# Optimization experiments

Hardware: AMD Instinct MI355X
Metric: run time of the kernel (lower is better)

Reference implementation:

```python
import jax, jax.numpy as jnp
import numpy as np

N_NODES = 1000000
N_EDGES = 32000000
NUM_GRAPHS = 1024


def setup_inputs() -> dict:
    key = jax.random.key(0)
    k1, k2, k3, k4, k5 = jax.random.split(key, 5)
    x = jax.random.normal(k1, (N_NODES, 1), dtype=jnp.float32)
    W = jax.random.normal(k2, (1, 1), dtype=jnp.float32)
    b = jax.random.normal(k3, (1,), dtype=jnp.float32)
    edge_index = jax.random.randint(k4, (2, N_EDGES), 0, N_NODES, dtype=jnp.int64)
    batch = jnp.sort(jax.random.randint(k5, (N_NODES,), 0, NUM_GRAPHS, dtype=jnp.int64))
    return {"x": x, "W": W, "b": b, "edge_index": edge_index, "batch": batch}


def reference(x, W, b, edge_index, batch):
    src, dst = edge_index[0], edge_index[1]
    # SimpleConv (default sum aggregation): out[i] = sum_{(j->i) in E} x[j]
    agg = jax.ops.segment_sum(x[src], dst, num_segments=N_NODES)  # [N,1]
    h = jax.nn.relu(agg)
    # global_mean_pool over graph ids
    sums = jax.ops.segment_sum(h, batch, num_segments=NUM_GRAPHS)  # [G,1]
    counts = jax.ops.segment_sum(jnp.ones((N_NODES,), dtype=h.dtype), batch,
                                 num_segments=NUM_GRAPHS)  # [G]
    pooled = sums / jnp.maximum(counts, 1.0)[:, None]
    # Linear(1 -> 1): y = pooled @ W^T + b
    return pooled @ W.T + b
```

## Files before the change

### kernel.cpp

```cpp
#include <hip/hip_runtime.h>

#define N_NODES    1000000
#define N_EDGES    32000000
#define NUM_GRAPHS 1024

typedef int          vint4  __attribute__((ext_vector_type(4)));
typedef unsigned int uint32;
typedef unsigned int vuint4 __attribute__((ext_vector_type(4)));

#define BUCKET_SHIFT 12
#define BUCKET_NODES (1 << BUCKET_SHIFT)
#define NBUCKETS     245

#define T1_NCHUNK   512
#define T1_BLOCK    512
#define T1_EDGES_PER_CHUNK (N_EDGES / T1_NCHUNK)
#define T1_QUADS    (T1_EDGES_PER_CHUNK / 4)
#define T1_ROUNDS   ((T1_QUADS + T1_BLOCK - 1) / T1_BLOCK)
#define SCAP        64
#define SLAB_CAP    368

#define RSPLIT        4
#define CELLS_PER_WG  (T1_NCHUNK / RSPLIT)

#define T2_CAP      136192
#define T2_NCHUNK   512
#define T2_EPC      (N_EDGES / T2_NCHUNK)

__global__ __launch_bounds__(T1_BLOCK)
void slab_scatter(const int* __restrict__ src,
                  const int* __restrict__ dst,
                  uint32* __restrict__ slab,
                  uint32* __restrict__ fcnt_g,
                  uint32* __restrict__ ecnt_g) {
    __shared__ uint32 stage[NBUCKETS][SCAP];
    __shared__ uint32 rpos[NBUCKETS];
    __shared__ uint32 ecnt[NBUCKETS];
    __shared__ uint32 flushed[NBUCKETS];
    __shared__ uint32 carry[NBUCKETS];

    const int tid = threadIdx.x;
    const int w   = blockIdx.x;
    const vint4* d4 = (const vint4*)(dst + (size_t)w * T1_EDGES_PER_CHUNK);
    const vint4* s4 = (const vint4*)(src + (size_t)w * T1_EDGES_PER_CHUNK);

    for (int b = tid; b < NBUCKETS; b += T1_BLOCK) {
        rpos[b] = 0; ecnt[b] = 0; flushed[b] = 0; carry[b] = 0;
    }
    __syncthreads();

    const int grp    = tid >> 4;
    const int lane16 = tid & 15;

    for (int r = 0; r < T1_ROUNDS; ++r) {
        int q = r * T1_BLOCK + tid;
        if (q < T1_QUADS) {
            vint4 d = d4[q];
            vint4 s = s4[q];
            #pragma unroll
            for (int k = 0; k < 4; ++k) {
                uint32 dd = (uint32)(k == 0 ? d.x : k == 1 ? d.y : k == 2 ? d.z : d.w);
                uint32 ss = (uint32)(k == 0 ? s.x : k == 1 ? s.y : k == 2 ? s.z : s.w);
                uint32 b  = dd >> BUCKET_SHIFT;
                uint32 v  = ((dd & (BUCKET_NODES - 1)) << 20) | ss;
                uint32 c  = carry[b] + atomicAdd(&rpos[b], 1u);
                if (c < SCAP) {
                    stage[b][c] = v;
                } else {
                    uint32 e = atomicAdd(&ecnt[b], 1u);
                    slab[((size_t)b * T1_NCHUNK + w) * SLAB_CAP + (SLAB_CAP - 1 - e)] = v;
                }
            }
        }
        __syncthreads();
        for (int b = grp; b < NBUCKETS; b += 32) {
            uint32 tot = carry[b] + rpos[b];
            if (tot > SCAP) tot = SCAP;
            uint32 lines = tot >> 4;
            uint32 rem   = tot & 15u;
            uint32 fl    = flushed[b];
            uint32* dp = slab + ((size_t)b * T1_NCHUNK + w) * SLAB_CAP + fl;
            for (uint32 l = 0; l < lines; ++l)
                dp[l * 16 + lane16] = stage[b][l * 16 + lane16];
            if (lines) {
                uint32 mv = 0;
                if (lane16 < rem) mv = stage[b][lines * 16 + lane16];
                if (lane16 < rem) stage[b][lane16] = mv;
            }
            if (lane16 == 0) {
                flushed[b] = fl + lines * 16;
                carry[b]   = rem;
                rpos[b]    = 0;
            }
        }
        __syncthreads();
    }
    for (int b = grp; b < NBUCKETS; b += 32) {
        uint32 rem = carry[b];
        uint32 fl  = flushed[b];
        uint32* dp = slab + ((size_t)b * T1_NCHUNK + w) * SLAB_CAP + fl;
        if (lane16 < rem) dp[lane16] = stage[b][lane16];
        if (lane16 == 0) {
            fcnt_g[(size_t)b * T1_NCHUNK + w] = fl + rem;
            ecnt_g[(size_t)b * T1_NCHUNK + w] = ecnt[b];
        }
    }
}

__global__ __launch_bounds__(1024)
void slab_reduce2(const uint32* __restrict__ slab,
                  const uint32* __restrict__ fcnt_g,
                  const uint32* __restrict__ ecnt_g,
                  const float* __restrict__ x,
                  float* __restrict__ agg) {
    __shared__ float  acc[BUCKET_NODES];
    __shared__ uint32 fc_s[CELLS_PER_WG];
    __shared__ uint32 ec_s[CELLS_PER_WG];

    const int b    = blockIdx.x / RSPLIT;
    const int part = blockIdx.x % RSPLIT;
    const int tid  = threadIdx.x;

    for (int n = tid; n < BUCKET_NODES; n += 1024) acc[n] = 0.0f;
    if (tid < CELLS_PER_WG) {
        size_t cell = (size_t)b * T1_NCHUNK + (size_t)part * CELLS_PER_WG + tid;
        fc_s[tid] = fcnt_g[cell];
        ec_s[tid] = ecnt_g[cell];
    }
    __syncthreads();

    const int wv = tid >> 6, lane = tid & 63;
    for (int c = wv; c < CELLS_PER_WG; c += 16) {
        const int w = part * CELLS_PER_WG + c;
        const size_t cell = (size_t)b * T1_NCHUNK + w;
        const uint32 fc = fc_s[c];
        const uint32 ec = ec_s[c];
        const uint32* base = slab + cell * SLAB_CAP;
        const vuint4* b4 = (const vuint4*)base;
        const uint32 nq = fc >> 2;
        for (uint32 i = lane; i < nq; i += 64) {
            vuint4 v = __builtin_nontemporal_load(&b4[i]);
            atomicAdd(&acc[v.x >> 20], x[v.x & 0xFFFFFu]);
            atomicAdd(&acc[v.y >> 20], x[v.y & 0xFFFFFu]);
            atomicAdd(&acc[v.z >> 20], x[v.z & 0xFFFFFu]);
            atomicAdd(&acc[v.w >> 20], x[v.w & 0xFFFFFu]);
        }
        for (uint32 i = nq * 4 + lane; i < fc; i += 64) {
            uint32 v = __builtin_nontemporal_load(&base[i]);
            atomicAdd(&acc[v >> 20], x[v & 0xFFFFFu]);
        }
        for (uint32 i = lane; i < ec; i += 64) {
            uint32 v = base[SLAB_CAP - 1 - i];
            atomicAdd(&acc[v >> 20], x[v & 0xFFFFFu]);
        }
    }
    __syncthreads();

    const int node0 = b << BUCKET_SHIFT;
    for (int n = tid; n < BUCKET_NODES; n += 1024) {
        float v = acc[n];
        if (v != 0.0f) atomicAdd(&agg[node0 + n], v);
    }
}

__global__ __launch_bounds__(1024)
void slab_reduce(const uint32* __restrict__ slab,
                 const uint32* __restrict__ fcnt_g,
                 const uint32* __restrict__ ecnt_g,
                 const float* __restrict__ x,
                 const int* __restrict__ batch,
                 float* __restrict__ sums,
                 float* __restrict__ counts) {
    __shared__ float acc[BUCKET_NODES];
    const int b = blockIdx.x;
    const int tid = threadIdx.x;
    for (int n = tid; n < BUCKET_NODES; n += 1024) acc[n] = 0.0f;
    __syncthreads();

    const int wv = tid >> 6, lane = tid & 63;
    for (int w = wv; w < T1_NCHUNK; w += 16) {
        size_t cell = (size_t)b * T1_NCHUNK + w;
        uint32 fc = fcnt_g[cell];
        uint32 ec = ecnt_g[cell];
        const uint32* base = slab + cell * SLAB_CAP;
        const vuint4* b4 = (const vuint4*)base;
        uint32 nq = fc >> 2;
        for (uint32 i = lane; i < nq; i += 64) {
            vuint4 v = b4[i];
            atomicAdd(&acc[v.x >> 20], x[v.x & 0xFFFFFu]);
            atomicAdd(&acc[v.y >> 20], x[v.y & 0xFFFFFu]);
            atomicAdd(&acc[v.z >> 20], x[v.z & 0xFFFFFu]);
            atomicAdd(&acc[v.w >> 20], x[v.w & 0xFFFFFu]);
        }
        for (uint32 i = nq * 4 + lane; i < fc; i += 64) {
            uint32 v = base[i];
            atomicAdd(&acc[v >> 20], x[v & 0xFFFFFu]);
        }
        for (uint32 i = lane; i < ec; i += 64) {
            uint32 v = base[SLAB_CAP - 1 - i];
            atomicAdd(&acc[v >> 20], x[v & 0xFFFFFu]);
        }
    }
    __syncthreads();

    const int node0 = b << BUCKET_SHIFT;
    for (int n = tid; n < BUCKET_NODES; n += 1024) {
        int i = node0 + n;
        float h = 0.0f;
        int g = -1;
        if (i < N_NODES) {
            h = fmaxf(acc[n], 0.0f);
            g = batch[i];
        }
        int g0 = __shfl(g, 0);
        if (__all(g == g0)) {
            #pragma unroll
            for (int off = 32; off > 0; off >>= 1)
                h += __shfl_down(h, off);
            if ((tid & 63) == 0 && g0 >= 0) {
                atomicAdd(&sums[g0], h);
                atomicAdd(&counts[g0], 64.0f);
            }
        } else if (g >= 0) {
            atomicAdd(&sums[g], h);
            atomicAdd(&counts[g], 1.0f);
        }
    }
}

__global__ void finalize_kernel(const float* __restrict__ sums,
                                const float* __restrict__ counts,
                                const float* __restrict__ W,
                                const float* __restrict__ b,
                                float* __restrict__ out) {
    int g = blockIdx.x * blockDim.x + threadIdx.x;
    if (g < NUM_GRAPHS) {
        float pooled = sums[g] / fmaxf(counts[g], 1.0f);
        out[g] = pooled * W[0] + b[0];
    }
}

__global__ __launch_bounds__(1024)
void bucket_scatter(const int* __restrict__ src,
                    const int* __restrict__ dst,
                    uint32* __restrict__ sorted,
                    uint32* __restrict__ gpos) {
    __shared__ uint32 hist[NBUCKETS];
    __shared__ uint32 pos[NBUCKETS];
    const int tid = threadIdx.x;
    const size_t base = (size_t)blockIdx.x * T2_EPC;
    for (int b = tid; b < NBUCKETS; b += 1024) hist[b] = 0;
    __syncthreads();
    const vint4* d4 = (const vint4*)(dst + base);
    const vint4* s4 = (const vint4*)(src + base);
    const int nvec = T2_EPC / 4;
    for (int i = tid; i < nvec; i += 1024) {
        vint4 d = d4[i];
        atomicAdd(&hist[(uint32)d.x >> BUCKET_SHIFT], 1u);
        atomicAdd(&hist[(uint32)d.y >> BUCKET_SHIFT], 1u);
        atomicAdd(&hist[(uint32)d.z >> BUCKET_SHIFT], 1u);
        atomicAdd(&hist[(uint32)d.w >> BUCKET_SHIFT], 1u);
    }
    __syncthreads();
    for (int b = tid; b < NBUCKETS; b += 1024)
        pos[b] = atomicAdd(&gpos[b], hist[b]);
    __syncthreads();
    for (int i = tid; i < nvec; i += 1024) {
        vint4 d = d4[i];
        vint4 s = s4[i];
        #pragma unroll
        for (int k = 0; k < 4; ++k) {
            uint32 dd = (uint32)(k == 0 ? d.x : k == 1 ? d.y : k == 2 ? d.z : d.w);
            uint32 ss = (uint32)(k == 0 ? s.x : k == 1 ? s.y : k == 2 ? s.z : s.w);
            uint32 b = dd >> BUCKET_SHIFT, dl = dd & (BUCKET_NODES - 1);
            uint32 slot = atomicAdd(&pos[b], 1u);
            if (slot < T2_CAP) sorted[(size_t)b * T2_CAP + slot] = (dl << 20) | ss;
        }
    }
}

__global__ __launch_bounds__(1024)
void bucket_reduce(const uint32* __restrict__ sorted,
                   const uint32* __restrict__ gpos,
                   const float* __restrict__ x,
                   const int* __restrict__ batch,
                   float* __restrict__ sums,
                   float* __restrict__ counts) {
    __shared__ float acc[BUCKET_NODES];
    const int b = blockIdx.x;
    const int tid = threadIdx.x;
    for (int n = tid; n < BUCKET_NODES; n += 1024) acc[n] = 0.0f;
    __syncthreads();
    uint32 cnt = gpos[b];
    if (cnt > T2_CAP) cnt = T2_CAP;
    const uint32* reg = sorted + (size_t)b * T2_CAP;
    const vuint4* r4 = (const vuint4*)reg;
    const uint32 nvec = cnt / 4;
    for (uint32 i = tid; i < nvec; i += 1024) {
        vuint4 v = r4[i];
        atomicAdd(&acc[v.x >> 20], x[v.x & 0xFFFFFu]);
        atomicAdd(&acc[v.y >> 20], x[v.y & 0xFFFFFu]);
        atomicAdd(&acc[v.z >> 20], x[v.z & 0xFFFFFu]);
        atomicAdd(&acc[v.w >> 20], x[v.w & 0xFFFFFu]);
    }
    for (uint32 i = nvec * 4 + tid; i < cnt; i += 1024) {
        uint32 v = reg[i];
        atomicAdd(&acc[v >> 20], x[v & 0xFFFFFu]);
    }
    __syncthreads();
    const int node0 = b << BUCKET_SHIFT;
    for (int n = tid; n < BUCKET_NODES; n += 1024) {
        int i = node0 + n;
        float h = 0.0f;
        int g = -1;
        if (i < N_NODES) {
            h = fmaxf(acc[n], 0.0f);
            g = batch[i];
        }
        int g0 = __shfl(g, 0);
        if (__all(g == g0)) {
            #pragma unroll
            for (int off = 32; off > 0; off >>= 1)
                h += __shfl_down(h, off);
            if ((tid & 63) == 0 && g0 >= 0) {
                atomicAdd(&sums[g0], h);
                atomicAdd(&counts[g0], 64.0f);
            }
        } else if (g >= 0) {
            atomicAdd(&sums[g], h);
            atomicAdd(&counts[g], 1.0f);
        }
    }
}

__global__ void scatter_edges_dev(const vint4* __restrict__ src4,
                                  const vint4* __restrict__ dst4,
                                  const float* __restrict__ x,
                                  float* __restrict__ agg) {
    int t = blockIdx.x * blockDim.x + threadIdx.x;
    if (t < N_EDGES / 4) {
        vint4 s = __builtin_nontemporal_load(&src4[t]);
        vint4 d = __builtin_nontemporal_load(&dst4[t]);
        atomicAdd(&agg[d.x], x[s.x]);
        atomicAdd(&agg[d.y], x[s.y]);
        atomicAdd(&agg[d.z], x[s.z]);
        atomicAdd(&agg[d.w], x[s.w]);
    }
}

__global__ void pool_nodes_kernel(const float* __restrict__ agg,
                                  const int* __restrict__ batch,
                                  float* __restrict__ sums,
                                  float* __restrict__ counts) {
    int i = blockIdx.x * blockDim.x + threadIdx.x;
    float h = 0.0f;
    int g = -1;
    if (i < N_NODES) {
        h = fmaxf(agg[i], 0.0f);
        g = batch[i];
    }
    int g0 = __shfl(g, 0);
    if (__all(g == g0)) {
        #pragma unroll
        for (int off = 32; off > 0; off >>= 1)
            h += __shfl_down(h, off);
        if ((threadIdx.x & 63) == 0 && g0 >= 0) {
            atomicAdd(&sums[g0], h);
            atomicAdd(&counts[g0], 64.0f);
        }
    } else if (g >= 0) {
        atomicAdd(&sums[g], h);
        atomicAdd(&counts[g], 1.0f);
    }
}

extern "C" void kernel_launch(void* const* d_in, const int* in_sizes, int n_in,
                              void* d_out, int out_size, void* d_ws, size_t ws_size,
                              hipStream_t stream) {
    const float* x     = (const float*)d_in[0];
    const float* W     = (const float*)d_in[1];
    const float* b     = (const float*)d_in[2];
    const int*   edge  = (const int*)d_in[3];
    const int*   batch = (const int*)d_in[4];
    float* out = (float*)d_out;

    const int* src = edge;
    const int* dst = edge + N_EDGES;

    const size_t ncells     = (size_t)NBUCKETS * T1_NCHUNK;
    const size_t slab_elems = ncells * SLAB_CAP;
    const size_t nagg       = (size_t)NBUCKETS * BUCKET_NODES;
    const size_t need0 = (slab_elems + 2 * ncells + nagg + 2 * NUM_GRAPHS) * 4;
    const size_t need1 = (slab_elems + 2 * ncells + 2 * NUM_GRAPHS) * 4;
    const size_t t2_elems = (size_t)NBUCKETS * T2_CAP;
    const size_t need2 = (t2_elems + 256 + 2 * NUM_GRAPHS) * 4;

    if (ws_size >= need0) {
        uint32* slab   = (uint32*)d_ws;
        uint32* fcnt_g = slab + slab_elems;
        uint32* ecnt_g = fcnt_g + ncells;
        float*  agg    = (float*)(ecnt_g + ncells);
        float*  sums   = agg + nagg;
        float*  counts = sums + NUM_GRAPHS;
        (void)hipMemsetAsync(agg, 0, (nagg + 2 * NUM_GRAPHS) * 4, stream);

        slab_scatter<<<T1_NCHUNK, T1_BLOCK, 0, stream>>>(src, dst, slab, fcnt_g, ecnt_g);
        slab_reduce2<<<NBUCKETS * RSPLIT, 1024, 0, stream>>>(slab, fcnt_g, ecnt_g, x, agg);
        pool_nodes_kernel<<<(N_NODES + 255) / 256, 256, 0, stream>>>(agg, batch, sums, counts);
        finalize_kernel<<<(NUM_GRAPHS + 255) / 256, 256, 0, stream>>>(sums, counts, W, b, out);
    } else if (ws_size >= need1) {
        uint32* slab   = (uint32*)d_ws;
        uint32* fcnt_g = slab + slab_elems;
        uint32* ecnt_g = fcnt_g + ncells;
        float*  sums   = (float*)(ecnt_g + ncells);
        float*  counts = sums + NUM_GRAPHS;
        (void)hipMemsetAsync(sums, 0, 2 * NUM_GRAPHS * 4, stream);

        slab_scatter<<<T1_NCHUNK, T1_BLOCK, 0, stream>>>(src, dst, slab, fcnt_g, ecnt_g);
        slab_reduce<<<NBUCKETS, 1024, 0, stream>>>(slab, fcnt_g, ecnt_g, x, batch, sums, counts);
        finalize_kernel<<<(NUM_GRAPHS + 255) / 256, 256, 0, stream>>>(sums, counts, W, b, out);
    } else if (ws_size >= need2) {
        uint32* sorted = (uint32*)d_ws;
        uint32* gpos   = sorted + t2_elems;
        float*  sums   = (float*)(gpos + 256);
        float*  counts = sums + NUM_GRAPHS;
        (void)hipMemsetAsync(gpos, 0, (256 + 2 * NUM_GRAPHS) * 4, stream);

        bucket_scatter<<<T2_NCHUNK, 1024, 0, stream>>>(src, dst, sorted, gpos);
        bucket_reduce<<<NBUCKETS, 1024, 0, stream>>>(sorted, gpos, x, batch, sums, counts);
        finalize_kernel<<<(NUM_GRAPHS + 255) / 256, 256, 0, stream>>>(sums, counts, W, b, out);
    } else {
        float* agg    = (float*)d_ws;
        float* sums   = agg + N_NODES;
        float* counts = sums + NUM_GRAPHS;
        (void)hipMemsetAsync(d_ws, 0, ((size_t)N_NODES + 2 * NUM_GRAPHS) * 4, stream);

        int nthreads = N_EDGES / 4;
        scatter_edges_dev<<<(nthreads + 255) / 256, 256, 0, stream>>>(
            (const vint4*)src, (const vint4*)dst, x, agg);
        pool_nodes_kernel<<<(N_NODES + 255) / 256, 256, 0, stream>>>(agg, batch, sums, counts);
        finalize_kernel<<<(NUM_GRAPHS + 255) / 256, 256, 0, stream>>>(sums, counts, W, b, out);
    }
}
```

Measured before the change: 650.1 us.

## Split reduce by source-node halves and use nontemporal loads/stores in scatter

The reduce kernel launches twice as many workgroups. Each one reads the whole slab cell but only gathers x values whose source index falls in its half of the node range, which shrinks the working set of x each workgroup touches so the random gathers stay in cache better. The scatter kernel switches its edge loads and slab stores to nontemporal hints so streaming traffic does not evict cached data. In exchange, every slab entry is now read twice and the extra range-check branches add divergence.

Result: slower. 692.5 us (+6.5%).

```diff
diff --git a/kernel.cpp b/kernel.cpp
--- a/kernel.cpp
+++ b/kernel.cpp
@@ -22,6 +22,8 @@
 
 #define RSPLIT        4
 #define CELLS_PER_WG  (T1_NCHUNK / RSPLIT)
+#define SRC_SPLIT     2
+#define HALF_NODES    (N_NODES / SRC_SPLIT)
 
 #define T2_CAP      136192
 #define T2_NCHUNK   512
@@ -55,8 +57,8 @@
     for (int r = 0; r < T1_ROUNDS; ++r) {
         int q = r * T1_BLOCK + tid;
         if (q < T1_QUADS) {
-            vint4 d = d4[q];
-            vint4 s = s4[q];
+            vint4 d = __builtin_nontemporal_load(&d4[q]);
+            vint4 s = __builtin_nontemporal_load(&s4[q]);
             #pragma unroll
             for (int k = 0; k < 4; ++k) {
                 uint32 dd = (uint32)(k == 0 ? d.x : k == 1 ? d.y : k == 2 ? d.z : d.w);
@@ -68,7 +70,8 @@
                     stage[b][c] = v;
                 } else {
                     uint32 e = atomicAdd(&ecnt[b], 1u);
-                    slab[((size_t)b * T1_NCHUNK + w) * SLAB_CAP + (SLAB_CAP - 1 - e)] = v;
+                    __builtin_nontemporal_store(v,
+                        &slab[((size_t)b * T1_NCHUNK + w) * SLAB_CAP + (SLAB_CAP - 1 - e)]);
                 }
             }
         }
@@ -81,7 +84,8 @@
             uint32 fl    = flushed[b];
             uint32* dp = slab + ((size_t)b * T1_NCHUNK + w) * SLAB_CAP + fl;
             for (uint32 l = 0; l < lines; ++l)
-                dp[l * 16 + lane16] = stage[b][l * 16 + lane16];
+                __builtin_nontemporal_store(stage[b][l * 16 + lane16],
+                                            &dp[l * 16 + lane16]);
             if (lines) {
                 uint32 mv = 0;
                 if (lane16 < rem) mv = stage[b][lines * 16 + lane16];
@@ -99,7 +103,7 @@
         uint32 rem = carry[b];
         uint32 fl  = flushed[b];
         uint32* dp = slab + ((size_t)b * T1_NCHUNK + w) * SLAB_CAP + fl;
-        if (lane16 < rem) dp[lane16] = stage[b][lane16];
+        if (lane16 < rem) __builtin_nontemporal_store(stage[b][lane16], &dp[lane16]);
         if (lane16 == 0) {
             fcnt_g[(size_t)b * T1_NCHUNK + w] = fl + rem;
             ecnt_g[(size_t)b * T1_NCHUNK + w] = ecnt[b];
@@ -117,9 +121,14 @@
     __shared__ uint32 fc_s[CELLS_PER_WG];
     __shared__ uint32 ec_s[CELLS_PER_WG];
 
-    const int b    = blockIdx.x / RSPLIT;
-    const int part = blockIdx.x % RSPLIT;
+    const int half = blockIdx.x & 1;
+    const int rest = blockIdx.x >> 1;
+    const int b    = rest / RSPLIT;
+    const int part = rest % RSPLIT;
     const int tid  = threadIdx.x;
+
+    const uint32 lo = (uint32)half * HALF_NODES;
+    const uint32 hi = lo + HALF_NODES;
 
     for (int n = tid; n < BUCKET_NODES; n += 1024) acc[n] = 0.0f;
     if (tid < CELLS_PER_WG) {
@@ -140,18 +149,22 @@
         const uint32 nq = fc >> 2;
         for (uint32 i = lane; i < nq; i += 64) {
             vuint4 v = __builtin_nontemporal_load(&b4[i]);
-            atomicAdd(&acc[v.x >> 20], x[v.x & 0xFFFFFu]);
-            atomicAdd(&acc[v.y >> 20], x[v.y & 0xFFFFFu]);
-            atomicAdd(&acc[v.z >> 20], x[v.z & 0xFFFFFu]);
-            atomicAdd(&acc[v.w >> 20], x[v.w & 0xFFFFFu]);
+            uint32 s0 = v.x & 0xFFFFFu, s1 = v.y & 0xFFFFFu;
+            uint32 s2 = v.z & 0xFFFFFu, s3 = v.w & 0xFFFFFu;
+            if (s0 >= lo && s0 < hi) atomicAdd(&acc[v.x >> 20], x[s0]);
+            if (s1 >= lo && s1 < hi) atomicAdd(&acc[v.y >> 20], x[s1]);
+            if (s2 >= lo && s2 < hi) atomicAdd(&acc[v.z >> 20], x[s2]);
+            if (s3 >= lo && s3 < hi) atomicAdd(&acc[v.w >> 20], x[s3]);
         }
         for (uint32 i = nq * 4 + lane; i < fc; i += 64) {
             uint32 v = __builtin_nontemporal_load(&base[i]);
-            atomicAdd(&acc[v >> 20], x[v & 0xFFFFFu]);
+            uint32 s = v & 0xFFFFFu;
+            if (s >= lo && s < hi) atomicAdd(&acc[v >> 20], x[s]);
         }
         for (uint32 i = lane; i < ec; i += 64) {
             uint32 v = base[SLAB_CAP - 1 - i];
-            atomicAdd(&acc[v >> 20], x[v & 0xFFFFFu]);
+            uint32 s = v & 0xFFFFFu;
+            if (s >= lo && s < hi) atomicAdd(&acc[v >> 20], x[s]);
         }
     }
     __syncthreads();
@@ -405,7 +418,8 @@
         (void)hipMemsetAsync(agg, 0, (nagg + 2 * NUM_GRAPHS) * 4, stream);
 
         slab_scatter<<<T1_NCHUNK, T1_BLOCK, 0, stream>>>(src, dst, slab, fcnt_g, ecnt_g);
-        slab_reduce2<<<NBUCKETS * RSPLIT, 1024, 0, stream>>>(slab, fcnt_g, ecnt_g, x, agg);
+        slab_reduce2<<<NBUCKETS * RSPLIT * SRC_SPLIT, 1024, 0, stream>>>(
+            slab, fcnt_g, ecnt_g, x, agg);
         pool_nodes_kernel<<<(N_NODES + 255) / 256, 256, 0, stream>>>(agg, batch, sums, counts);
         finalize_kernel<<<(NUM_GRAPHS + 255) / 256, 256, 0, stream>>>(sums, counts, W, b, out);
     } else if (ws_size >= need1) {
```
